# Kernel optimization log

Hardware: AMD Instinct MI355X
Metric: run time of the kernel (lower is better)

## Reference

```python
import jax, jax.numpy as jnp
import numpy as np


def _adaptive_pool_mat(n_in, n_out):
    # torch AdaptiveAvgPool2d bin edges: start=floor(i*n_in/n_out), end=ceil((i+1)*n_in/n_out)
    M = np.zeros((n_out, n_in), np.float32)
    for i in range(n_out):
        s = (i * n_in) // n_out
        e = -(-((i + 1) * n_in) // n_out)
        M[i, s:e] = 1.0 / (e - s)
    return jnp.asarray(M)


def _bilinear_mat(n_out, n_in):
    # torch F.interpolate bilinear, align_corners=False, as a (n_out, n_in) matrix
    M = np.zeros((n_out, n_in), np.float32)
    scale = n_in / n_out
    for i in range(n_out):
        src = max((i + 0.5) * scale - 0.5, 0.0)
        i0 = min(int(np.floor(src)), n_in - 1)
        w = src - i0
        i1 = min(i0 + 1, n_in - 1)
        M[i, i0] += 1.0 - w
        M[i, i1] += w
    return jnp.asarray(M)


def _bn(x, g, b, m, v):
    # inference-mode BatchNorm2d over channel axis 1 of (B,C,H,W)
    inv = g / jnp.sqrt(v + 1e-5)
    return x * inv[None, :, None, None] + (b - m * inv)[None, :, None, None]


def _selective_scan(u, delta, A, Bs, Cs, D):
    # u, delta: (B,K,Di,L); A: (K,Di,N); Bs, Cs: (B,K,N,L); D: (K,Di)
    def step(h, inp):
        u_l, d_l, B_l, C_l = inp  # (B,K,Di), (B,K,Di), (B,K,N), (B,K,N)
        h = h * jnp.exp(d_l[..., None] * A) + (d_l * u_l)[..., None] * B_l[:, :, None, :]
        return h, jnp.einsum('bkdn,bkn->bkd', h, C_l)

    h0 = jnp.zeros(u.shape[:3] + (A.shape[-1],), u.dtype)
    xs = (u.transpose(3, 0, 1, 2), delta.transpose(3, 0, 1, 2),
          Bs.transpose(3, 0, 1, 2), Cs.transpose(3, 0, 1, 2))
    _, ys = jax.lax.scan(step, h0, xs)  # ys: (L,B,K,Di)
    return ys.transpose(1, 2, 3, 0) + D[None, :, :, None] * u


def _ss2d(x, in_proj_w, conv_w, conv_b, x_proj_w, dt_w, dt_b, A_logs, Ds, ln_g, ln_b, out_proj_w):
    # x: (B,H,W,d_model); VMamba SS2D with K=4 scan directions
    B, H, W, _ = x.shape
    K, N = 4, 16
    R = dt_w.shape[-1]
    Di = in_proj_w.shape[0] // 2
    xz = jnp.einsum('bhwc,ec->bhwe', x, in_proj_w)
    xi, z = jnp.split(xz, 2, axis=-1)
    xc = xi.transpose(0, 3, 1, 2)  # (B,Di,H,W)
    xc = jax.lax.conv_general_dilated(xc, conv_w, (1, 1), [(1, 1), (1, 1)],
                                      dimension_numbers=('NCHW', 'OIHW', 'NCHW'),
                                      feature_group_count=Di)
    xc = jax.nn.silu(xc + conv_b[None, :, None, None])
    L = H * W
    x_hw = xc.reshape(B, Di, L)
    x_wh = xc.transpose(0, 1, 3, 2).reshape(B, Di, L)
    xs2 = jnp.stack([x_hw, x_wh], axis=1)
    xs4 = jnp.concatenate([xs2, jnp.flip(xs2, axis=-1)], axis=1)  # (B,4,Di,L)
    x_dbl = jnp.einsum('bkdl,kcd->bkcl', xs4, x_proj_w)
    dts, Bm, Cm = jnp.split(x_dbl, [R, R + N], axis=2)
    delta = jax.nn.softplus(jnp.einsum('bkrl,kdr->bkdl', dts, dt_w) + dt_b[None, :, :, None])
    A = -jnp.exp(A_logs).reshape(K, Di, N)
    out_y = _selective_scan(xs4, delta, A, Bm, Cm, Ds.reshape(K, Di))  # (B,4,Di,L)
    inv_y = jnp.flip(out_y[:, 2:4], axis=-1)
    wh_y = out_y[:, 1].reshape(B, Di, W, H).transpose(0, 1, 3, 2).reshape(B, Di, L)
    invwh_y = inv_y[:, 1].reshape(B, Di, W, H).transpose(0, 1, 3, 2).reshape(B, Di, L)
    y = out_y[:, 0] + inv_y[:, 0] + wh_y + invwh_y  # (B,Di,L)
    y = y.transpose(0, 2, 1).reshape(B, H, W, Di)
    mu = jnp.mean(y, -1, keepdims=True)
    var = jnp.var(y, -1, keepdims=True)
    y = (y - mu) / jnp.sqrt(var + 1e-5) * ln_g + ln_b  # out_norm (LayerNorm)
    y = y * jax.nn.silu(z)
    return jnp.einsum('bhwd,cd->bhwc', y, out_proj_w)


def _forward(x, pool_w, pool_b, bn_g, bn_b, bn_m, bn_v, in_proj_w, conv_w, conv_b,
             x_proj_w, dt_w, dt_b, A_logs, Ds, ln_g, ln_b, out_proj_w,
             cbr_w, cbr_b, cbr_g, cbr_beta, cbr_m, cbr_v):
    B, C, H, W = x.shape
    pool_scales = [1, 5, 9, 13]  # generate_arithmetic_sequence(1, 16, 4)
    outs = [x]
    # pool layer 0: conv1x1 -> BN -> ReLU -> global avg pool -> upsample (constant)
    y0 = jnp.einsum('bchw,dc->bdhw', x, pool_w[0]) + pool_b[0][None, :, None, None]
    y0 = jax.nn.relu(_bn(y0, bn_g[0], bn_b[0], bn_m[0], bn_v[0]))
    y0 = jnp.mean(y0, axis=(2, 3), keepdims=True)
    outs.append(jnp.broadcast_to(y0, (B, y0.shape[1], H, W)))
    # pool layers 1..3: adaptive avg pool -> conv1x1 -> BN -> ReLU -> bilinear upsample
    for i, s in enumerate(pool_scales[1:], start=1):
        Mh, Mw = _adaptive_pool_mat(H, s), _adaptive_pool_mat(W, s)
        p = jnp.einsum('bchw,ph,qw->bcpq', x, Mh, Mw)
        p = jnp.einsum('bcpq,dc->bdpq', p, pool_w[i]) + pool_b[i][None, :, None, None]
        p = jax.nn.relu(_bn(p, bn_g[i], bn_b[i], bn_m[i], bn_v[i]))
        Uh, Uw = _bilinear_mat(H, s), _bilinear_mat(W, s)
        outs.append(jnp.einsum('bcpq,hp,wq->bchw', p, Uh, Uw))
    feat = jnp.concatenate(outs, axis=1)  # (B, dim*4 + in_chs = 1024, H, W)
    y = _ss2d(feat.transpose(0, 2, 3, 1), in_proj_w, conv_w, conv_b, x_proj_w,
              dt_w, dt_b, A_logs, Ds, ln_g, ln_b, out_proj_w)
    y = y.transpose(0, 3, 1, 2)
    # cbr: conv1x1 -> BN -> GELU
    y = jnp.einsum('bchw,dc->bdhw', y, cbr_w) + cbr_b[None, :, None, None]
    y = _bn(y, cbr_g, cbr_beta, cbr_m, cbr_v)
    return jax.nn.gelu(y, approximate=False)


def setup_inputs():
    key = jax.random.key(0)
    ks = jax.random.split(key, 20)
    B, C, H, W = 4, 512, 16, 16
    dim, P = 128, 4
    dm = dim * P + C            # 1024
    Di, K, N, R = 2 * dm, 4, 16, dm // 16  # 2048, 4, 16, 64
    f = jax.random.normal
    return {
        'x': f(ks[0], (B, C, H, W), jnp.float32),
        'pool_w': f(ks[1], (P, dim, C), jnp.float32) * 0.05,
        'pool_b': f(ks[2], (P, dim), jnp.float32) * 0.05,
        'bn_g': jnp.ones((P, dim), jnp.float32),
        'bn_b': jnp.zeros((P, dim), jnp.float32),
        'bn_m': f(ks[3], (P, dim), jnp.float32) * 0.1,
        'bn_v': jax.random.uniform(ks[4], (P, dim), jnp.float32, 0.5, 1.5),
        'in_proj_w': f(ks[5], (2 * Di, dm), jnp.float32) * 0.02,
        'conv_w': f(ks[6], (Di, 1, 3, 3), jnp.float32) * 0.1,
        'conv_b': f(ks[7], (Di,), jnp.float32) * 0.05,
        'x_proj_w': f(ks[8], (K, R + 2 * N, Di), jnp.float32) * 0.02,
        'dt_w': f(ks[9], (K, Di, R), jnp.float32) * 0.05,
        'dt_b': f(ks[10], (K, Di), jnp.float32) * 0.1,
        'A_logs': jax.random.uniform(ks[11], (K * Di, N), jnp.float32),
        'Ds': f(ks[12], (K * Di,), jnp.float32) * 0.1,
        'ln_g': jnp.ones((Di,), jnp.float32),
        'ln_b': jnp.zeros((Di,), jnp.float32),
        'out_proj_w': f(ks[13], (dm, Di), jnp.float32) * 0.02,
        'cbr_w': f(ks[14], (dim, dm), jnp.float32) * 0.05,
        'cbr_b': f(ks[15], (dim,), jnp.float32) * 0.05,
        'cbr_g': jnp.ones((dim,), jnp.float32),
        'cbr_beta': jnp.zeros((dim,), jnp.float32),
        'cbr_m': f(ks[16], (dim,), jnp.float32) * 0.1,
        'cbr_v': jax.random.uniform(ks[17], (dim,), jnp.float32, 0.5, 1.5),
    }


def reference(x, pool_w, pool_b, bn_g, bn_b, bn_m, bn_v, in_proj_w, conv_w, conv_b,
              x_proj_w, dt_w, dt_b, A_logs, Ds, ln_g, ln_b, out_proj_w,
              cbr_w, cbr_b, cbr_g, cbr_beta, cbr_m, cbr_v):
    return _forward(x, pool_w, pool_b, bn_g, bn_b, bn_m, bn_v, in_proj_w, conv_w, conv_b,
                    x_proj_w, dt_w, dt_b, A_logs, Ds, ln_g, ln_b, out_proj_w,
                    cbr_w, cbr_b, cbr_g, cbr_beta, cbr_m, cbr_v)
```

## Files before the change

### kernel.cpp

```cpp
#include <hip/hip_runtime.h>
#include <hip/hip_bf16.h>
#include <math.h>

#define Bsz 4
#define Cin 512
#define Hh 16
#define Ww 16
#define Lsp 256
#define DIM 128
#define DM 1024
#define DI 2048
#define KK 4
#define NST 16
#define RR 64
#define PW 384
#define NCH 4
#define CHUNK 64

#define OFF_FEAT    0u
#define SZ_FEAT     (Bsz*Lsp*DM)
#define OFF_POOLED  (OFF_FEAT + SZ_FEAT)
#define SZ_POOLED   (Bsz*Cin*275)
#define OFF_PCONV   (OFF_POOLED + SZ_POOLED)
#define SZ_PCONV    (Bsz*275*DIM)
#define OFF_Y0M     (OFF_PCONV + SZ_PCONV)
#define SZ_Y0M      (Bsz*DIM)
#define OFF_XZ      (OFF_Y0M + SZ_Y0M)
#define SZ_XZ       (Bsz*Lsp*2*DI)
#define OFF_XCT     (OFF_XZ + SZ_XZ)
#define SZ_XCT      (Bsz*Lsp*DI)
#define OFF_XDBL    (OFF_XCT + SZ_XCT)
#define SZ_XDBL     (Bsz*Lsp*PW)
#define OFF_DELTA   (OFF_XDBL + SZ_XDBL)
#define SZ_DELTA    (Bsz*KK*Lsp*DI)
#define OFF_OUTY    (OFF_DELTA + SZ_DELTA)
#define SZ_OUTY     (Bsz*KK*Lsp*DI)
#define OFF_YG      (OFF_OUTY + SZ_OUTY)
#define SZ_YG       (Bsz*Lsp*DI)
#define OFF_O1      (OFF_YG + SZ_YG)
#define SZ_O1       (Bsz*Lsp*DM)
#define OFF_O2      (OFF_O1 + SZ_O1)
#define SZ_O2       (Bsz*Lsp*DIM)
#define WS_FLOATS   (OFF_O2 + SZ_O2)

typedef __attribute__((ext_vector_type(8))) short short8;
typedef __attribute__((ext_vector_type(4))) float f32x4;

__device__ __forceinline__ short f2bf(float x) {
  __hip_bfloat16 h = __float2bfloat16(x);
  short s;
  __builtin_memcpy(&s, &h, 2);
  return s;
}
__device__ __forceinline__ float bf2f(short s) {
  unsigned u = ((unsigned)(unsigned short)s) << 16;
  float f;
  __builtin_memcpy(&f, &u, 4);
  return f;
}
__device__ __forceinline__ float unpack_lo(unsigned v) {
  unsigned u = v << 16; float f; __builtin_memcpy(&f, &u, 4); return f;
}
__device__ __forceinline__ float unpack_hi(unsigned v) {
  unsigned u = v & 0xffff0000u; float f; __builtin_memcpy(&f, &u, 4); return f;
}

__global__ __launch_bounds__(256) void f2bf5_kernel(
    const float* __restrict__ s0, short* __restrict__ d0,
    const float* __restrict__ s1, short* __restrict__ d1,
    const float* __restrict__ s2, short* __restrict__ d2,
    const float* __restrict__ s3, short* __restrict__ d3,
    const float* __restrict__ s4, short* __restrict__ d4) {
  int blk = blockIdx.x;
  const float* src; short* dst; int base;
  if (blk < 2048)      { src = s0; dst = d0; base = blk; }
  else if (blk < 2432) { src = s1; dst = d1; base = blk - 2048; }
  else if (blk < 3456) { src = s2; dst = d2; base = blk - 2432; }
  else if (blk < 3520) { src = s3; dst = d3; base = blk - 3456; }
  else                 { src = s4; dst = d4; base = blk - 3520; }
  int i = (base*256 + threadIdx.x)*8;
  float4 a = *(const float4*)(src + i);
  float4 b = *(const float4*)(src + i + 4);
  short8 o;
  o[0]=f2bf(a.x); o[1]=f2bf(a.y); o[2]=f2bf(a.z); o[3]=f2bf(a.w);
  o[4]=f2bf(b.x); o[5]=f2bf(b.y); o[6]=f2bf(b.z); o[7]=f2bf(b.w);
  *(short8*)(dst + i) = o;
}

__global__ __launch_bounds__(256) void pool0_kernel(
    const float* __restrict__ x, const float* __restrict__ pw, const float* __restrict__ pb,
    const float* __restrict__ g, const float* __restrict__ bb,
    const float* __restrict__ m, const float* __restrict__ v, float* __restrict__ y0m) {
  int bd = blockIdx.x;
  int b = bd >> 7, d = bd & 127;
  int l = threadIdx.x;
  const float* xb = x + (b*Cin)*Lsp + l;
  const float* w = pw + d*Cin;
  float a0 = 0.f, a1 = 0.f, a2 = 0.f, a3 = 0.f;
  #pragma unroll 4
  for (int c = 0; c < Cin; c += 4) {
    float4 wv = *(const float4*)(w + c);
    a0 += xb[(c+0)*Lsp] * wv.x;
    a1 += xb[(c+1)*Lsp] * wv.y;
    a2 += xb[(c+2)*Lsp] * wv.z;
    a3 += xb[(c+3)*Lsp] * wv.w;
  }
  float s = (a0 + a1) + (a2 + a3) + pb[d];
  float inv = g[d] * rsqrtf(v[d] + 1e-5f);
  s = s*inv + (bb[d] - m[d]*inv);
  s = fmaxf(s, 0.f);
  __shared__ float red[256];
  red[l] = s; __syncthreads();
  for (int off = 128; off > 0; off >>= 1) {
    if (l < off) red[l] += red[l+off];
    __syncthreads();
  }
  if (l == 0) y0m[bd] = red[0] * (1.f/256.f);
}

__device__ __forceinline__ void decode_pos(int pos, int& s, int& pp, int& qq, int& layer) {
  if (pos < 25)       { s = 5;  layer = 1; int t = pos;       pp = t/5;  qq = t%5;  }
  else if (pos < 106) { s = 9;  layer = 2; int t = pos - 25;  pp = t/9;  qq = t%9;  }
  else                { s = 13; layer = 3; int t = pos - 106; pp = t/13; qq = t%13; }
}

__global__ void pool_avg_kernel(const float* __restrict__ x, float* __restrict__ pooled) {
  int bc = blockIdx.x;
  int pos = threadIdx.x;
  if (pos >= 275) return;
  int s, pp, qq, layer;
  decode_pos(pos, s, pp, qq, layer);
  int hs = (pp*Hh)/s, he = ((pp+1)*Hh + s-1)/s;
  int ws = (qq*Ww)/s, we = ((qq+1)*Ww + s-1)/s;
  const float* xb = x + (size_t)bc*Lsp;
  float acc = 0.f;
  for (int hh = hs; hh < he; ++hh)
    for (int ww2 = ws; ww2 < we; ++ww2)
      acc += xb[hh*Ww + ww2];
  pooled[(size_t)bc*275 + pos] = acc / (float)((he-hs)*(we-ws));
}

__global__ void pconv_kernel(const float* __restrict__ pooled, const float* __restrict__ pw,
    const float* __restrict__ pb, const float* __restrict__ g, const float* __restrict__ bb,
    const float* __restrict__ m, const float* __restrict__ v, float* __restrict__ pconv) {
  int bp = blockIdx.x;
  int b = bp / 275, pos = bp % 275;
  int d = threadIdx.x;
  int s, pp, qq, layer;
  decode_pos(pos, s, pp, qq, layer);
  const float* pc = pooled + b*Cin*275 + pos;
  const float* w = pw + (layer*DIM + d)*Cin;
  float a0 = 0.f, a1 = 0.f, a2 = 0.f, a3 = 0.f;
  #pragma unroll 4
  for (int c = 0; c < Cin; c += 4) {
    float4 wv = *(const float4*)(w + c);
    a0 += pc[(c+0)*275] * wv.x;
    a1 += pc[(c+1)*275] * wv.y;
    a2 += pc[(c+2)*275] * wv.z;
    a3 += pc[(c+3)*275] * wv.w;
  }
  float acc = (a0 + a1) + (a2 + a3) + pb[layer*DIM + d];
  int ld = layer*DIM + d;
  float inv = g[ld] * rsqrtf(v[ld] + 1e-5f);
  acc = acc*inv + (bb[ld] - m[ld]*inv);
  pconv[bp*DIM + d] = fmaxf(acc, 0.f);
}

__global__ __launch_bounds__(256) void xT_kernel(const float* __restrict__ x,
    short* __restrict__ featB) {
  int b = blockIdx.z;
  int c0 = blockIdx.x*32, l0 = blockIdx.y*32;
  __shared__ float t[32][33];
  int tx = threadIdx.x & 31, ty = threadIdx.x >> 5;
  #pragma unroll
  for (int i = 0; i < 4; ++i) {
    int c = c0 + ty + i*8;
    t[ty + i*8][tx] = x[((size_t)b*Cin + c)*Lsp + l0 + tx];
  }
  __syncthreads();
  #pragma unroll
  for (int i = 0; i < 4; ++i) {
    int l = l0 + ty + i*8;
    featB[(size_t)(b*Lsp + l)*DM + c0 + tx] = f2bf(t[tx][ty + i*8]);
  }
}

__global__ __launch_bounds__(256) void feat_fill(const float* __restrict__ y0m,
    const float* __restrict__ pconv, short* __restrict__ featB) {
  int bl = blockIdx.x;
  int b = bl >> 8, l = bl & 255;
  int h = l >> 4, w = l & 15;
  for (int cc = threadIdx.x; cc < 512; cc += 256) {
    float val;
    if (cc < 128) {
      val = y0m[b*DIM + cc];
    } else {
      int i = (cc - 128) >> 7;
      int d = (cc - 128) & 127;
      int s = (i==0) ? 5 : (i==1) ? 9 : 13;
      int off = (i==0) ? 0 : (i==1) ? 25 : 106;
      float scale = (float)s / 16.f;
      float sh = fmaxf((h + 0.5f)*scale - 0.5f, 0.f);
      int h0 = min((int)sh, s-1); float wh = sh - (float)h0; int h1 = min(h0+1, s-1);
      float sw = fmaxf((w + 0.5f)*scale - 0.5f, 0.f);
      int w0 = min((int)sw, s-1); float ww2 = sw - (float)w0; int w1 = min(w0+1, s-1);
      const float* pc = pconv + b*275*DIM;
      float v00 = pc[(off + h0*s + w0)*DIM + d];
      float v01 = pc[(off + h0*s + w1)*DIM + d];
      float v10 = pc[(off + h1*s + w0)*DIM + d];
      float v11 = pc[(off + h1*s + w1)*DIM + d];
      val = (1.f-wh)*((1.f-ww2)*v00 + ww2*v01) + wh*((1.f-ww2)*v10 + ww2*v11);
    }
    featB[(size_t)bl*DM + 512 + cc] = f2bf(val);
  }
}

__device__ __forceinline__ int dir_map(int k, int l) {
  if (k == 0) return l;
  if (k == 1) return ((l & 15) << 4) | (l >> 4);
  if (k == 2) return 255 - l;
  int m = 255 - l; return ((m & 15) << 4) | (m >> 4);
}
__device__ __forceinline__ int inv_map(int k, int sp) {
  int t = ((sp & 15) << 4) | (sp >> 4);
  if (k == 0) return sp;
  if (k == 1) return t;
  if (k == 2) return 255 - sp;
  return 255 - t;
}

__device__ __forceinline__ void gload_lds16(const short* g, short* l) {
  __builtin_amdgcn_global_load_lds((const __attribute__((address_space(1))) void*)g,
                                   (__attribute__((address_space(3))) void*)l, 16, 0, 0);
}

template<int MODE>
__global__ __launch_bounds__(256) void gemm_bf(const short* __restrict__ Ag,
    const short* __restrict__ Bg, void* __restrict__ Cout, const float* __restrict__ bias,
    int M, int N, int K, int lda, int ldb,
    int azs, int bzs, unsigned czs, int ezs,
    const short* __restrict__ xcb, void* __restrict__ aux) {
  __shared__ short Als[128*64];
  __shared__ short Bls[128*64];
  int kdir = blockIdx.z;
  Ag += (size_t)kdir * azs;
  Bg += (size_t)kdir * bzs;
  size_t cz = (size_t)kdir * czs;
  if (bias) bias += (size_t)kdir * ezs;
  int tid = threadIdx.x;
  int w = tid >> 6, lane = tid & 63;
  int wm = w >> 1, wn = w & 1;
  int row0 = blockIdx.y * 128, col0 = blockIdx.x * 128;
  f32x4 acc[4][4];
  #pragma unroll
  for (int i = 0; i < 4; ++i)
    #pragma unroll
    for (int j = 0; j < 4; ++j)
      acc[i][j] = (f32x4){0.f, 0.f, 0.f, 0.f};

  for (int k0 = 0; k0 < K; k0 += 64) {
    #pragma unroll
    for (int i = 0; i < 4; ++i) {
      int slot = i*256 + w*64 + lane;
      int r = slot >> 3, pc = slot & 7;
      int c = pc ^ (r & 7);
      gload_lds16(Ag + (size_t)(row0 + r)*lda + k0 + c*8, &Als[(i*256 + w*64)*8]);
      gload_lds16(Bg + (size_t)(col0 + r)*ldb + k0 + c*8, &Bls[(i*256 + w*64)*8]);
    }
    __syncthreads();
    #pragma unroll
    for (int ks = 0; ks < 2; ++ks) {
      short8 af[4], bfr[4];
      int rsel = lane & 15, csel = ks*4 + (lane >> 4);
      #pragma unroll
      for (int mi = 0; mi < 4; ++mi) {
        int row = wm*64 + mi*16 + rsel;
        af[mi] = *(const short8*)&Als[row*64 + ((csel ^ (row & 7)) << 3)];
      }
      #pragma unroll
      for (int ni = 0; ni < 4; ++ni) {
        int row = wn*64 + ni*16 + rsel;
        bfr[ni] = *(const short8*)&Bls[row*64 + ((csel ^ (row & 7)) << 3)];
      }
      #pragma unroll
      for (int mi = 0; mi < 4; ++mi)
        #pragma unroll
        for (int ni = 0; ni < 4; ++ni)
          acc[mi][ni] = __builtin_amdgcn_mfma_f32_16x16x32_bf16(af[mi], bfr[ni], acc[mi][ni], 0, 0, 0);
    }
    __syncthreads();
  }
  #pragma unroll
  for (int mi = 0; mi < 4; ++mi) {
    int rbase = row0 + wm*64 + mi*16 + ((lane >> 4) << 2);
    #pragma unroll
    for (int ni = 0; ni < 4; ++ni) {
      int colg = col0 + wn*64 + ni*16 + (lane & 15);
      #pragma unroll
      for (int j = 0; j < 4; ++j) {
        if (MODE == 1) {
          ((short*)Cout)[(size_t)(rbase + j)*N + colg] = f2bf(acc[mi][ni][j]);
        } else if (MODE == 4) {
          int rowg = rbase + j;
          int b_ = rowg >> 8, sp_ = rowg & 255;
          int lsc = inv_map(kdir, sp_);
          float dl = acc[mi][ni][j] + bias[colg];
          dl = (dl > 20.f) ? dl : __logf(1.f + __expf(dl));
          float ul = bf2f(xcb[(size_t)rowg*N + colg]);
          unsigned pv = ((unsigned)(unsigned short)f2bf(dl*ul) << 16)
                      |  (unsigned)(unsigned short)f2bf(dl);
          ((unsigned*)Cout)[cz + (size_t)(b_*Lsp + lsc)*N + colg] = pv;
        } else if (MODE == 5) {
          float vv = acc[mi][ni][j];
          ((float*)Cout)[(size_t)(rbase + j)*N + colg] = vv;
          ((short*)aux)[(size_t)(rbase + j)*N + colg] = f2bf(vv);
        } else {
          ((float*)Cout)[(size_t)(rbase + j)*N + colg] = acc[mi][ni][j];
        }
      }
    }
  }
}

__global__ __launch_bounds__(256) void dwconv_kernel(const short* __restrict__ xzB,
    const float* __restrict__ cw, const float* __restrict__ cb, short* __restrict__ xcB) {
  int bl = blockIdx.x;
  int b = bl >> 8, l = bl & 255;
  int h = l >> 4, w = l & 15;
  const short* xzb = xzB + (size_t)b*Lsp*(2*DI);
  #pragma unroll
  for (int it = 0; it < 4; ++it) {
    int d = (threadIdx.x + it*256)*2;
    float s0 = cb[d], s1 = cb[d+1];
    #pragma unroll
    for (int dh = -1; dh <= 1; ++dh) {
      int hh = h + dh; if (hh < 0 || hh > 15) continue;
      #pragma unroll
      for (int dw = -1; dw <= 1; ++dw) {
        int ww2 = w + dw; if (ww2 < 0 || ww2 > 15) continue;
        int t = (dh+1)*3 + (dw+1);
        short2 xv = *(const short2*)&xzb[(size_t)(hh*16 + ww2)*(2*DI) + d];
        s0 += bf2f(xv.x) * cw[d*9 + t];
        s1 += bf2f(xv.y) * cw[(d+1)*9 + t];
      }
    }
    float r0 = s0 / (1.f + __expf(-s0));
    float r1 = s1 / (1.f + __expf(-s1));
    short2 o; o.x = f2bf(r0); o.y = f2bf(r1);
    *(short2*)&xcB[((size_t)b*Lsp + l)*DI + d] = o;
  }
}

__global__ __launch_bounds__(256) void ps_build(const float* __restrict__ P,
    float* __restrict__ PS) {
  int slab = blockIdx.x;
  int k = slab >> 2, b = slab & 3;
  int l = threadIdx.x;
  int sp = dir_map(k, l);
  const float* src = P + (size_t)(b*Lsp + sp)*PW + k*96 + RR;
  float* dst = PS + ((size_t)slab*Lsp + l)*32;
  #pragma unroll
  for (int n = 0; n < 32; n += 4)
    *(float4*)(dst + n) = *(const float4*)(src + n);
}

__global__ __launch_bounds__(256) void scan_fused(const unsigned* __restrict__ pk,
    const float* __restrict__ PS, const float* __restrict__ A_logs,
    short* __restrict__ oyB) {
  int bk = blockIdx.x;
  int b = bk >> 2, k = bk & 3;
  int slab = k*Bsz + b;
  int tid = threadIdx.x;
  int wv = tid >> 6, lane = tid & 63;
  int dloc = lane >> 2, ng = lane & 3;
  int d = blockIdx.y*16 + dloc;
  int n0 = ng*4;
  __shared__ float sHend[3][16][16];
  __shared__ float sPa[2][16][16];
  float A[4];
  #pragma unroll
  for (int j = 0; j < 4; ++j)
    A[j] = -__expf(A_logs[((size_t)k*DI + d)*NST + n0 + j]);
  const unsigned* pkp = pk + (size_t)slab*Lsp*DI;
  const float* ps  = PS + (size_t)slab*Lsp*32;
  short* oy = oyB + (size_t)bk*Lsp*DI;
  float h[4] = {0.f,0.f,0.f,0.f};

  if (wv == 0) {
    #pragma unroll 2
    for (int l = 0; l < CHUNK; ++l) {
      unsigned v = pkp[(size_t)l*DI + d];
      float dl = unpack_lo(v);
      float du = unpack_hi(v);
      float4 Bv = *(const float4*)(ps + l*32 + n0);
      float4 Cv = *(const float4*)(ps + l*32 + 16 + n0);
      float y;
      float e0 = __expf(dl*A[0]); h[0] = h[0]*e0 + du*Bv.x; y  = h[0]*Cv.x;
      float e1 = __expf(dl*A[1]); h[1] = h[1]*e1 + du*Bv.y; y += h[1]*Cv.y;
      float e2 = __expf(dl*A[2]); h[2] = h[2]*e2 + du*Bv.z; y += h[2]*Cv.z;
      float e3 = __expf(dl*A[3]); h[3] = h[3]*e3 + du*Bv.w; y += h[3]*Cv.w;
      y += __shfl_xor(y, 1);
      y += __shfl_xor(y, 2);
      if (ng == 0) oy[(size_t)l*DI + d] = f2bf(y);
    }
    #pragma unroll
    for (int j = 0; j < 4; ++j) sHend[0][dloc][n0+j] = h[j];
  } else if (wv <= 2) {
    int c = wv;
    float sdl = 0.f;
    #pragma unroll 2
    for (int l = c*CHUNK; l < (c+1)*CHUNK; ++l) {
      unsigned v = pkp[(size_t)l*DI + d];
      float dl = unpack_lo(v);
      float du = unpack_hi(v);
      sdl += dl;
      float4 Bv = *(const float4*)(ps + l*32 + n0);
      float e0 = __expf(dl*A[0]); h[0] = h[0]*e0 + du*Bv.x;
      float e1 = __expf(dl*A[1]); h[1] = h[1]*e1 + du*Bv.y;
      float e2 = __expf(dl*A[2]); h[2] = h[2]*e2 + du*Bv.z;
      float e3 = __expf(dl*A[3]); h[3] = h[3]*e3 + du*Bv.w;
    }
    #pragma unroll
    for (int j = 0; j < 4; ++j) {
      sHend[c][dloc][n0+j] = h[j];
      sPa[c-1][dloc][n0+j] = __expf(A[j]*sdl);
    }
  } else {
    unsigned ua = 0u; float fa = 0.f;
    for (int l = 3*CHUNK; l < 4*CHUNK; l += 2) {
      ua += pkp[(size_t)l*DI + d];
      fa += ps[l*32 + (lane & 31)];
    }
    asm volatile("" :: "v"(ua), "v"(fa));
  }
  __syncthreads();
  if (wv >= 1) {
    int c = wv;
    #pragma unroll
    for (int j = 0; j < 4; ++j) {
      float hh = sHend[0][dloc][n0+j];
      if (c >= 2) hh = sPa[0][dloc][n0+j]*hh + sHend[1][dloc][n0+j];
      if (c == 3) hh = sPa[1][dloc][n0+j]*hh + sHend[2][dloc][n0+j];
      h[j] = hh;
    }
    #pragma unroll 2
    for (int l = c*CHUNK; l < (c+1)*CHUNK; ++l) {
      unsigned v = pkp[(size_t)l*DI + d];
      float dl = unpack_lo(v);
      float du = unpack_hi(v);
      float4 Bv = *(const float4*)(ps + l*32 + n0);
      float4 Cv = *(const float4*)(ps + l*32 + 16 + n0);
      float y;
      float e0 = __expf(dl*A[0]); h[0] = h[0]*e0 + du*Bv.x; y  = h[0]*Cv.x;
      float e1 = __expf(dl*A[1]); h[1] = h[1]*e1 + du*Bv.y; y += h[1]*Cv.y;
      float e2 = __expf(dl*A[2]); h[2] = h[2]*e2 + du*Bv.z; y += h[2]*Cv.z;
      float e3 = __expf(dl*A[3]); h[3] = h[3]*e3 + du*Bv.w; y += h[3]*Cv.w;
      y += __shfl_xor(y, 1);
      y += __shfl_xor(y, 2);
      if (ng == 0) oy[(size_t)l*DI + d] = f2bf(y);
    }
  }
}

__global__ __launch_bounds__(256) void combine_ln_kernel(const short* __restrict__ oyB,
    const short* __restrict__ xzB, const short* __restrict__ xcB,
    const float* __restrict__ Ds, const float* __restrict__ lng,
    const float* __restrict__ lnb, short* __restrict__ ygB) {
  int bl = blockIdx.x;
  int b = bl >> 8, l = bl & 255;
  int h = l >> 4, w = l & 15;
  int lT = (w << 4) | h;
  const short* oy = oyB + (size_t)b*KK*Lsp*DI;
  float vals[8];
  float sum = 0.f, sumsq = 0.f;
  #pragma unroll
  for (int i = 0; i < 8; ++i) {
    int d = threadIdx.x + i*256;
    float dsum = Ds[d] + Ds[DI + d] + Ds[2*DI + d] + Ds[3*DI + d];
    float yv = bf2f(oy[(size_t)(0*Lsp + l       )*DI + d])
             + bf2f(oy[(size_t)(2*Lsp + (255-l ))*DI + d])
             + bf2f(oy[(size_t)(1*Lsp + lT      )*DI + d])
             + bf2f(oy[(size_t)(3*Lsp + (255-lT))*DI + d])
             + bf2f(xcB[(size_t)bl*DI + d]) * dsum;
    vals[i] = yv; sum += yv; sumsq += yv*yv;
  }
  __shared__ float r1[256], r2[256];
  r1[threadIdx.x] = sum; r2[threadIdx.x] = sumsq; __syncthreads();
  for (int off = 128; off > 0; off >>= 1) {
    if (threadIdx.x < off) { r1[threadIdx.x] += r1[threadIdx.x+off]; r2[threadIdx.x] += r2[threadIdx.x+off]; }
    __syncthreads();
  }
  float mu = r1[0] * (1.f/2048.f);
  float var = r2[0] * (1.f/2048.f) - mu*mu;
  float rstd = rsqrtf(var + 1e-5f);
  const short* zrow = xzB + (size_t)bl*(2*DI) + DI;
  #pragma unroll
  for (int i = 0; i < 8; ++i) {
    int d = threadIdx.x + i*256;
    float z = bf2f(zrow[d]);
    float sz = z / (1.f + __expf(-z));
    ygB[(size_t)bl*DI + d] = f2bf(((vals[i]-mu)*rstd*lng[d] + lnb[d]) * sz);
  }
}

__global__ void cbr_epilogue(const float* __restrict__ o2, const float* __restrict__ cb,
    const float* __restrict__ g, const float* __restrict__ beta, const float* __restrict__ m_,
    const float* __restrict__ v_, float* __restrict__ out) {
  int idx = blockIdx.x*256 + threadIdx.x;
  int l = idx & 255;
  int rest = idx >> 8;
  int dd = rest & 127;
  int b = rest >> 7;
  float s = o2[((size_t)b*Lsp + l)*DIM + dd] + cb[dd];
  float inv = g[dd] * rsqrtf(v_[dd] + 1e-5f);
  s = s*inv + (beta[dd] - m_[dd]*inv);
  out[idx] = s * 0.5f * (1.f + erff(s * 0.70710678118f));
}

extern "C" void kernel_launch(void* const* d_in, const int* in_sizes, int n_in,
                              void* d_out, int out_size, void* d_ws, size_t ws_size,
                              hipStream_t stream) {
  const float* x        = (const float*)d_in[0];
  const float* pool_w   = (const float*)d_in[1];
  const float* pool_b   = (const float*)d_in[2];
  const float* bn_g     = (const float*)d_in[3];
  const float* bn_b     = (const float*)d_in[4];
  const float* bn_m     = (const float*)d_in[5];
  const float* bn_v     = (const float*)d_in[6];
  const float* in_proj_w= (const float*)d_in[7];
  const float* conv_w   = (const float*)d_in[8];
  const float* conv_b   = (const float*)d_in[9];
  const float* x_proj_w = (const float*)d_in[10];
  const float* dt_w     = (const float*)d_in[11];
  const float* dt_b     = (const float*)d_in[12];
  const float* A_logs   = (const float*)d_in[13];
  const float* Ds       = (const float*)d_in[14];
  const float* ln_g     = (const float*)d_in[15];
  const float* ln_b     = (const float*)d_in[16];
  const float* out_proj_w=(const float*)d_in[17];
  const float* cbr_w    = (const float*)d_in[18];
  const float* cbr_b    = (const float*)d_in[19];
  const float* cbr_g    = (const float*)d_in[20];
  const float* cbr_beta = (const float*)d_in[21];
  const float* cbr_m    = (const float*)d_in[22];
  const float* cbr_v    = (const float*)d_in[23];
  float* out = (float*)d_out;

  if (ws_size < (size_t)WS_FLOATS * sizeof(float)) return;
  float* ws = (float*)d_ws;
  float* pooled   = ws + OFF_POOLED;
  float* pconv    = ws + OFF_PCONV;
  float* y0m      = ws + OFF_Y0M;
  float* P        = ws + OFF_XDBL;
  unsigned* pk    = (unsigned*)(ws + OFF_DELTA);
  float* o2       = ws + OFF_O2;

  short* featB = (short*)(ws + OFF_POOLED);
  float* PS    = ws + OFF_POOLED;
  short* xzB   = (short*)(ws + OFF_XZ);
  short* wInB  = (short*)(ws + OFF_DELTA);
  short* wXB   = (short*)(ws + OFF_DELTA + 2097152);
  short* wOB   = (short*)(ws + OFF_FEAT);
  short* wCB   = (short*)(ws + OFF_PCONV);
  short* xcB   = (short*)(ws + OFF_O1);
  short* oyB   = (short*)(ws + OFF_OUTY);
  short* dtwB  = (short*)(ws + OFF_OUTY + 4194304);
  short* PB    = (short*)(ws + OFF_OUTY + 4194304 + 262144);
  short* ygB   = (short*)(ws + OFF_DELTA);
  short* o1B   = (short*)(ws + OFF_O1);

  pool0_kernel<<<Bsz*DIM, 256, 0, stream>>>(x, pool_w, pool_b, bn_g, bn_b, bn_m, bn_v, y0m);
  pool_avg_kernel<<<Bsz*Cin, 288, 0, stream>>>(x, pooled);
  pconv_kernel<<<Bsz*275, 128, 0, stream>>>(pooled, pool_w, pool_b, bn_g, bn_b, bn_m, bn_v, pconv);
  xT_kernel<<<dim3(16, 8, Bsz), 256, 0, stream>>>(x, featB);
  feat_fill<<<Bsz*Lsp, 256, 0, stream>>>(y0m, pconv, featB);

  f2bf5_kernel<<<3776, 256, 0, stream>>>(in_proj_w, wInB, x_proj_w, wXB,
      out_proj_w, wOB, cbr_w, wCB, dt_w, dtwB);

  gemm_bf<1><<<dim3(32, 8, 1), 256, 0, stream>>>(featB, wInB, xzB, nullptr,
      1024, 4096, 1024, 1024, 1024, 0, 0, 0, 0, nullptr, nullptr);

  dwconv_kernel<<<Bsz*Lsp, 256, 0, stream>>>(xzB, conv_w, conv_b, xcB);

  gemm_bf<5><<<dim3(3, 8, 1), 256, 0, stream>>>(xcB, wXB, P, nullptr,
      1024, PW, 2048, 2048, 2048, 0, 0, 0, 0, nullptr, PB);
  ps_build<<<16, 256, 0, stream>>>(P, PS);

  gemm_bf<4><<<dim3(16, 8, KK), 256, 0, stream>>>(PB, dtwB, pk, dt_b,
      1024, DI, 64, PW, RR, 96, DI*RR, (unsigned)(Bsz*Lsp*DI), DI, xcB, nullptr);

  scan_fused<<<dim3(Bsz*KK, DI/16), 256, 0, stream>>>(pk, PS, A_logs, oyB);

  combine_ln_kernel<<<Bsz*Lsp, 256, 0, stream>>>(oyB, xzB, xcB, Ds, ln_g, ln_b, ygB);

  gemm_bf<1><<<dim3(8, 8, 1), 256, 0, stream>>>(ygB, wOB, o1B, nullptr,
      1024, 1024, 2048, 2048, 2048, 0, 0, 0, 0, nullptr, nullptr);

  gemm_bf<0><<<dim3(1, 8, 1), 256, 0, stream>>>(o1B, wCB, o2, nullptr,
      1024, DIM, 1024, 1024, 1024, 0, 0, 0, 0, nullptr, nullptr);
  cbr_epilogue<<<(Bsz*DIM*Lsp)/256, 256, 0, stream>>>(o2, cbr_b, cbr_g, cbr_beta, cbr_m, cbr_v, out);
}
```

Baseline: 317.3 us.

## Give each scan lane a full channel with all 16 states in registers

The selective-scan kernel now maps one lane to one channel d and keeps all 16 state values in registers, where before 4 lanes each held 4 states. This removes the two cross-lane shuffle reductions and the redundant pk loads per channel, and each block now covers 64 channels, so the grid shrinks fourfold. In exchange each thread uses more registers, the B/C values are read as uniform scalar loads, and there are fewer blocks, so occupancy and latency hiding may drop. The prefetch warp also touches fewer rows.

```diff
diff --git a/kernel.cpp b/kernel.cpp
--- a/kernel.cpp
+++ b/kernel.cpp
@@ -372,92 +372,81 @@
   int slab = k*Bsz + b;
   int tid = threadIdx.x;
   int wv = tid >> 6, lane = tid & 63;
-  int dloc = lane >> 2, ng = lane & 3;
-  int d = blockIdx.y*16 + dloc;
-  int n0 = ng*4;
-  __shared__ float sHend[3][16][16];
-  __shared__ float sPa[2][16][16];
-  float A[4];
-  #pragma unroll
-  for (int j = 0; j < 4; ++j)
-    A[j] = -__expf(A_logs[((size_t)k*DI + d)*NST + n0 + j]);
+  int d = blockIdx.y*64 + lane;
+  __shared__ float sH[3][64][17];
+  __shared__ float sPa[2][64][17];
+  float A[16], h[16];
+  #pragma unroll
+  for (int n = 0; n < 16; ++n) {
+    A[n] = -__expf(A_logs[((size_t)k*DI + d)*NST + n]);
+    h[n] = 0.f;
+  }
   const unsigned* pkp = pk + (size_t)slab*Lsp*DI;
   const float* ps  = PS + (size_t)slab*Lsp*32;
   short* oy = oyB + (size_t)bk*Lsp*DI;
-  float h[4] = {0.f,0.f,0.f,0.f};
 
   if (wv == 0) {
-    #pragma unroll 2
     for (int l = 0; l < CHUNK; ++l) {
       unsigned v = pkp[(size_t)l*DI + d];
-      float dl = unpack_lo(v);
-      float du = unpack_hi(v);
-      float4 Bv = *(const float4*)(ps + l*32 + n0);
-      float4 Cv = *(const float4*)(ps + l*32 + 16 + n0);
-      float y;
-      float e0 = __expf(dl*A[0]); h[0] = h[0]*e0 + du*Bv.x; y  = h[0]*Cv.x;
-      float e1 = __expf(dl*A[1]); h[1] = h[1]*e1 + du*Bv.y; y += h[1]*Cv.y;
-      float e2 = __expf(dl*A[2]); h[2] = h[2]*e2 + du*Bv.z; y += h[2]*Cv.z;
-      float e3 = __expf(dl*A[3]); h[3] = h[3]*e3 + du*Bv.w; y += h[3]*Cv.w;
-      y += __shfl_xor(y, 1);
-      y += __shfl_xor(y, 2);
-      if (ng == 0) oy[(size_t)l*DI + d] = f2bf(y);
-    }
-    #pragma unroll
-    for (int j = 0; j < 4; ++j) sHend[0][dloc][n0+j] = h[j];
+      float dl = unpack_lo(v), du = unpack_hi(v);
+      const float* pr = ps + l*32;
+      float y = 0.f;
+      #pragma unroll
+      for (int n = 0; n < 16; ++n) {
+        float e = __expf(dl*A[n]);
+        h[n] = h[n]*e + du*pr[n];
+        y += h[n]*pr[16+n];
+      }
+      oy[(size_t)l*DI + d] = f2bf(y);
+    }
+    #pragma unroll
+    for (int n = 0; n < 16; ++n) sH[0][lane][n] = h[n];
   } else if (wv <= 2) {
     int c = wv;
     float sdl = 0.f;
-    #pragma unroll 2
     for (int l = c*CHUNK; l < (c+1)*CHUNK; ++l) {
       unsigned v = pkp[(size_t)l*DI + d];
-      float dl = unpack_lo(v);
-      float du = unpack_hi(v);
+      float dl = unpack_lo(v), du = unpack_hi(v);
+      const float* pr = ps + l*32;
       sdl += dl;
-      float4 Bv = *(const float4*)(ps + l*32 + n0);
-      float e0 = __expf(dl*A[0]); h[0] = h[0]*e0 + du*Bv.x;
-      float e1 = __expf(dl*A[1]); h[1] = h[1]*e1 + du*Bv.y;
-      float e2 = __expf(dl*A[2]); h[2] = h[2]*e2 + du*Bv.z;
-      float e3 = __expf(dl*A[3]); h[3] = h[3]*e3 + du*Bv.w;
-    }
-    #pragma unroll
-    for (int j = 0; j < 4; ++j) {
-      sHend[c][dloc][n0+j] = h[j];
-      sPa[c-1][dloc][n0+j] = __expf(A[j]*sdl);
+      #pragma unroll
+      for (int n = 0; n < 16; ++n) {
+        float e = __expf(dl*A[n]);
+        h[n] = h[n]*e + du*pr[n];
+      }
+    }
+    #pragma unroll
+    for (int n = 0; n < 16; ++n) {
+      sH[c][lane][n] = h[n];
+      sPa[c-1][lane][n] = __expf(A[n]*sdl);
     }
   } else {
-    unsigned ua = 0u; float fa = 0.f;
-    for (int l = 3*CHUNK; l < 4*CHUNK; l += 2) {
-      ua += pkp[(size_t)l*DI + d];
-      fa += ps[l*32 + (lane & 31)];
-    }
-    asm volatile("" :: "v"(ua), "v"(fa));
+    unsigned ua = 0u;
+    for (int l = 3*CHUNK; l < 4*CHUNK; l += 4) ua += pkp[(size_t)l*DI + d];
+    asm volatile("" :: "v"(ua));
   }
   __syncthreads();
   if (wv >= 1) {
     int c = wv;
     #pragma unroll
-    for (int j = 0; j < 4; ++j) {
-      float hh = sHend[0][dloc][n0+j];
-      if (c >= 2) hh = sPa[0][dloc][n0+j]*hh + sHend[1][dloc][n0+j];
-      if (c == 3) hh = sPa[1][dloc][n0+j]*hh + sHend[2][dloc][n0+j];
-      h[j] = hh;
-    }
-    #pragma unroll 2
+    for (int n = 0; n < 16; ++n) {
+      float hh = sH[0][lane][n];
+      if (c >= 2) hh = sPa[0][lane][n]*hh + sH[1][lane][n];
+      if (c == 3) hh = sPa[1][lane][n]*hh + sH[2][lane][n];
+      h[n] = hh;
+    }
     for (int l = c*CHUNK; l < (c+1)*CHUNK; ++l) {
       unsigned v = pkp[(size_t)l*DI + d];
-      float dl = unpack_lo(v);
-      float du = unpack_hi(v);
-      float4 Bv = *(const float4*)(ps + l*32 + n0);
-      float4 Cv = *(const float4*)(ps + l*32 + 16 + n0);
-      float y;
-      float e0 = __expf(dl*A[0]); h[0] = h[0]*e0 + du*Bv.x; y  = h[0]*Cv.x;
-      float e1 = __expf(dl*A[1]); h[1] = h[1]*e1 + du*Bv.y; y += h[1]*Cv.y;
-      float e2 = __expf(dl*A[2]); h[2] = h[2]*e2 + du*Bv.z; y += h[2]*Cv.z;
-      float e3 = __expf(dl*A[3]); h[3] = h[3]*e3 + du*Bv.w; y += h[3]*Cv.w;
-      y += __shfl_xor(y, 1);
-      y += __shfl_xor(y, 2);
-      if (ng == 0) oy[(size_t)l*DI + d] = f2bf(y);
+      float dl = unpack_lo(v), du = unpack_hi(v);
+      const float* pr = ps + l*32;
+      float y = 0.f;
+      #pragma unroll
+      for (int n = 0; n < 16; ++n) {
+        float e = __expf(dl*A[n]);
+        h[n] = h[n]*e + du*pr[n];
+        y += h[n]*pr[16+n];
+      }
+      oy[(size_t)l*DI + d] = f2bf(y);
     }
   }
 }
@@ -590,7 +579,7 @@
   gemm_bf<4><<<dim3(16, 8, KK), 256, 0, stream>>>(PB, dtwB, pk, dt_b,
       1024, DI, 64, PW, RR, 96, DI*RR, (unsigned)(Bsz*Lsp*DI), DI, xcB, nullptr);
 
-  scan_fused<<<dim3(Bsz*KK, DI/16), 256, 0, stream>>>(pk, PS, A_logs, oyB);
+  scan_fused<<<dim3(Bsz*KK, DI/64), 256, 0, stream>>>(pk, PS, A_logs, oyB);
 
   combine_ln_kernel<<<Bsz*Lsp, 256, 0, stream>>>(oyB, xzB, xcB, Ds, ln_g, ln_b, ygB);
 
```

Measured after the change: 340.4 us. 1.07x slower.
